# Kernel tuning notes

Hardware: AMD Instinct MI355X
Metric: run time of the kernel (lower is better)

The kernel has to match this reference:

```python
import jax, jax.numpy as jnp
import numpy as np

CHUNK = 2048  # query chunk for KNN to avoid materializing full [B,N,N] distances
BN_EPS = 1e-5


def knn_idx(xyz, k):
    """xyz: [B,N,3] -> idx [B,N,k] of k nearest points (incl. self), like keops argKmin."""
    B, N, _ = xyz.shape
    nc = N // CHUNK
    qs = jnp.moveaxis(xyz.reshape(B, nc, CHUNK, 3), 1, 0)  # [nc,B,CHUNK,3]

    def chunk_fn(q):  # q: [B,CHUNK,3]
        d = jnp.sum((q[:, :, None, :] - xyz[:, None, :, :]) ** 2, axis=-1)  # [B,CHUNK,N]
        _, idx = jax.lax.top_k(-d, k)
        return idx

    idx = jax.lax.map(chunk_fn, qs)  # [nc,B,CHUNK,k]
    return jnp.moveaxis(idx, 0, 1).reshape(B, N, k)


def setup_inputs() -> dict:
    key = jax.random.key(0)
    k1, k2, k3, k4 = jax.random.split(key, 4)
    B, N, C = 4, 16384, 128
    return {
        "xyz": jax.random.normal(k1, (B, N, 3), dtype=jnp.float32),
        "x": jax.random.normal(k2, (B, C, N), dtype=jnp.float32),
        "conv_w": jax.random.normal(k3, (C, C), dtype=jnp.float32) * (1.0 / np.sqrt(C)),
        "conv_b": jax.random.normal(k4, (C,), dtype=jnp.float32) * 0.01,
        "gamma": jnp.ones((C,), dtype=jnp.float32),
        "beta": jnp.zeros((C,), dtype=jnp.float32),
        "k": 16,
    }


def reference(xyz, x, conv_w, conv_b, gamma, beta, k):
    # KNN on coordinates
    idx = knn_idx(xyz, k)                       # [B,N,k]
    xt = jnp.swapaxes(x, 1, 2)                  # [B,N,C]
    neigh = jax.vmap(lambda p, i: p[i])(xt, idx)  # [B,N,k,C] gather per batch
    # dx = sum over k neighbors minus center feature (Laplacian-like)
    dx = jnp.swapaxes(neigh.sum(axis=2) - xt, 1, 2)  # [B,C,N]
    # conv1x1 -> relu -> batchnorm (training-mode batch stats) -> residual
    h = jax.nn.relu(jnp.einsum('oc,bcn->bon', conv_w, dx) + conv_b[None, :, None])
    mean = h.mean(axis=(0, 2))
    var = h.var(axis=(0, 2))  # biased variance, as torch BN normalization
    hn = (h - mean[None, :, None]) * jax.lax.rsqrt(var[None, :, None] + BN_EPS)
    return x + gamma[None, :, None] * hn + beta[None, :, None]
```

## Files before the change

kernel.cpp:

```cpp
#include <hip/hip_runtime.h>

#define BATCH 4
#define NPTS  16384
#define CH    128
#define KNN   16

#define G      64
#define GRID3  (G * G * G)
#define GW     0.25f
#define GINVW  4.0f
#define GORIG  (-8.0f)
#define OCCW   (GRID3 / 32)

#define XT_OFF    0
#define HT_OFF    33554432
#define CNT_OFF   33554432
#define CUR_OFF   37748736
#define HDR_OFF   41943040
#define OCC_OFF   50331648
#define SPTS_OFF  50462720
#define GCTR_OFF  51511296
#define IDX_OFF   67108864
#define PART_OFF  71303168
#define STATS_OFF 75497472

__device__ __forceinline__ int cell1(float v) {
    int c = (int)floorf((v - GORIG) * GINVW);
    return min(G - 1, max(0, c));
}

__global__ __launch_bounds__(256) void zero_kernel(int* __restrict__ p, int n,
                                                   int* __restrict__ gctr) {
    int i = blockIdx.x * 256 + threadIdx.x;
    if (i < BATCH) gctr[i] = 0;
    const int stride = gridDim.x * 256;
    for (; i < n; i += stride) p[i] = 0;
}

__global__ __launch_bounds__(256) void transpose_kernel(const float* __restrict__ x,
                                                        float* __restrict__ xt) {
    __shared__ float t[32][33];
    const int b  = blockIdx.z;
    const int c0 = blockIdx.y * 32;
    const int n0 = blockIdx.x * 32;
    const int tx = threadIdx.x, ty = threadIdx.y;
#pragma unroll
    for (int i = 0; i < 4; ++i)
        t[ty + 8 * i][tx] = x[((size_t)b * CH + c0 + ty + 8 * i) * NPTS + n0 + tx];
    __syncthreads();
#pragma unroll
    for (int i = 0; i < 4; ++i)
        xt[((size_t)b * NPTS + n0 + ty + 8 * i) * CH + c0 + tx] = t[tx][ty + 8 * i];
}

__global__ __launch_bounds__(256) void count_kernel(const float* __restrict__ xyz,
                                                    int* __restrict__ counts) {
    const int b = blockIdx.y;
    const int i = blockIdx.x * 256 + threadIdx.x;
    const float* p = xyz + ((size_t)b * NPTS + i) * 3;
    const int c = (cell1(p[2]) * G + cell1(p[1])) * G + cell1(p[0]);
    atomicAdd(&counts[(size_t)b * GRID3 + c], 1);
}

__global__ __launch_bounds__(256) void cellhdr_kernel(const int* __restrict__ counts,
                                                      int2* __restrict__ hdr,
                                                      unsigned int* __restrict__ occ,
                                                      int* __restrict__ gctr) {
    const int cid  = blockIdx.x * 256 + threadIdx.x;
    const int b    = cid >> 18;
    const int lane = threadIdx.x & 63;
    const int c    = counts[cid];

    int incl = c;
#pragma unroll
    for (int off = 1; off < 64; off <<= 1) {
        int t = __shfl_up(incl, off);
        if (lane >= off) incl += t;
    }
    const int excl = incl - c;
    const int tot  = __shfl(incl, 63);

    const unsigned long long ball = __ballot(c > 0);
    if (lane == 0) {
        const int w = cid >> 5;
        occ[w]     = (unsigned int)ball;
        occ[w + 1] = (unsigned int)(ball >> 32);
    }

    int base = 0;
    if (lane == 63) base = atomicAdd(&gctr[b], tot);
    base = __shfl(base, 63);

    if (c > 0) hdr[cid] = make_int2(base + excl, c);
}

__global__ __launch_bounds__(256) void scatter_kernel(const float* __restrict__ xyz,
                                                      const int2* __restrict__ hdr,
                                                      int* __restrict__ cursor,
                                                      float4* __restrict__ spts) {
    const int b = blockIdx.y;
    const int i = blockIdx.x * 256 + threadIdx.x;
    const float* p = xyz + ((size_t)b * NPTS + i) * 3;
    const float x = p[0], y = p[1], z = p[2];
    const int c = (cell1(z) * G + cell1(y)) * G + cell1(x);
    const int pos = hdr[(size_t)b * GRID3 + c].x + atomicAdd(&cursor[(size_t)b * GRID3 + c], 1);
    spts[(size_t)b * NPTS + pos] = make_float4(x, y, z, __int_as_float(i));
}

__global__ __launch_bounds__(256) void knn_grid_kernel(const float4* __restrict__ spts,
                                                       const int2* __restrict__ hdr,
                                                       const unsigned int* __restrict__ occ,
                                                       int* __restrict__ idx_out) {
    __shared__ unsigned int socc[OCCW];
    const int b   = blockIdx.y;
    const int tid = threadIdx.x;
    for (int i = tid; i < OCCW; i += 256) socc[i] = occ[(size_t)b * OCCW + i];
    __syncthreads();

    const int s = blockIdx.x * 256 + tid;
    const float4 P = spts[(size_t)b * NPTS + s];
    const float qx = P.x, qy = P.y, qz = P.z;
    const int qi = __float_as_int(P.w);
    const int cx = cell1(qx), cy = cell1(qy), cz = cell1(qz);
    const int2* hb = hdr + (size_t)b * GRID3;
    const float4* pts = spts + (size_t)b * NPTS;

    float dq[KNN]; int iq[KNN];
#pragma unroll
    for (int t = 0; t < KNN; ++t) { dq[t] = 3.0e38f; iq[t] = 0x7fffffff; }

    for (int R = 0; R < G; ++R) {
        if (R > 0) {
            const int rm = R - 1;
            float dmin = 3.0e38f;
            bool any = false;
            if (cx - rm > 0)     { dmin = fminf(dmin, qx - (GORIG + (cx - rm) * GW)); any = true; }
            if (cx + rm < G - 1) { dmin = fminf(dmin, (GORIG + (cx + rm + 1) * GW) - qx); any = true; }
            if (cy - rm > 0)     { dmin = fminf(dmin, qy - (GORIG + (cy - rm) * GW)); any = true; }
            if (cy + rm < G - 1) { dmin = fminf(dmin, (GORIG + (cy + rm + 1) * GW) - qy); any = true; }
            if (cz - rm > 0)     { dmin = fminf(dmin, qz - (GORIG + (cz - rm) * GW)); any = true; }
            if (cz + rm < G - 1) { dmin = fminf(dmin, (GORIG + (cz + rm + 1) * GW) - qz); any = true; }
            if (!any) break;
            dmin = fmaxf(dmin, 0.0f);
            if (dq[KNN - 1] < dmin * dmin * (1.0f - 1e-5f)) break;
        }
        const int z0 = max(0, cz - R), z1 = min(G - 1, cz + R);
        const int y0 = max(0, cy - R), y1 = min(G - 1, cy + R);
        const int x0 = max(0, cx - R), x1 = min(G - 1, cx + R);
        for (int z = z0; z <= z1; ++z) {
            const int az = (z > cz) ? (z - cz) : (cz - z);
            const float lz = GORIG + z * GW;
            const float dzc = fmaxf(fmaxf(lz - qz, qz - (lz + GW)), 0.0f);
            for (int y = y0; y <= y1; ++y) {
                const int ay = (y > cy) ? (y - cy) : (cy - y);
                const float ly = GORIG + y * GW;
                const float dyc = fmaxf(fmaxf(ly - qy, qy - (ly + GW)), 0.0f);
                const float dzy = dzc * dzc + dyc * dyc;
                const int row = z * G + y;

                unsigned long long m;
                if (az == R || ay == R) {
                    m = (~0ull >> (63 - (x1 - x0))) << x0;
                } else {
                    m = 0ull;
                    if (cx - R >= 0) m |= 1ull << (cx - R);
                    if (cx + R < G)  m |= 1ull << (cx + R);
                }
                m &= (unsigned long long)socc[row * 2] |
                     ((unsigned long long)socc[row * 2 + 1] << 32);

                while (m) {
                    const int x = __ffsll(m) - 1;
                    m &= m - 1;
                    const float lx = GORIG + x * GW;
                    const float dxc = fmaxf(fmaxf(lx - qx, qx - (lx + GW)), 0.0f);
                    const float cmin = dzy + dxc * dxc;
                    if (cmin * (1.0f - 1e-5f) > dq[KNN - 1]) continue;
                    const int2 hc = hb[row * G + x];
                    const int en = hc.x + hc.y;
                    for (int j = hc.x; j < en; ++j) {
                        const float4 pp = pts[j];
                        const float ddx = __fsub_rn(qx, pp.x);
                        const float ddy = __fsub_rn(qy, pp.y);
                        const float ddz = __fsub_rn(qz, pp.z);
                        const float d = __fadd_rn(__fadd_rn(__fmul_rn(ddx, ddx), __fmul_rn(ddy, ddy)),
                                                  __fmul_rn(ddz, ddz));
                        const int oi = __float_as_int(pp.w);
                        if (d < dq[KNN - 1] || (d == dq[KNN - 1] && oi < iq[KNN - 1])) {
                            float cd = d; int ci = oi;
#pragma unroll
                            for (int t2 = KNN - 1; t2 >= 1; --t2) {
                                const bool lt = (cd < dq[t2 - 1]) ||
                                                (cd == dq[t2 - 1] && ci < iq[t2 - 1]);
                                if (lt) {
                                    dq[t2] = dq[t2 - 1]; iq[t2] = iq[t2 - 1];
                                    if (t2 == 1) { dq[0] = cd; iq[0] = ci; }
                                } else {
                                    dq[t2] = cd; iq[t2] = ci;
                                    break;
                                }
                            }
                        }
                    }
                }
            }
        }
    }

    int* op = idx_out + ((size_t)b * NPTS + qi) * KNN;
#pragma unroll
    for (int t = 0; t < KNN; ++t) op[t] = iq[t];
}

__global__ __launch_bounds__(128) void conv_kernel(const float* __restrict__ xt,
                                                   const int* __restrict__ idx,
                                                   const float* __restrict__ W,
                                                   const float* __restrict__ bias,
                                                   float* __restrict__ h_t,
                                                   float* __restrict__ partials) {
    __shared__ __align__(16) float dxbuf[CH];
    const int o   = threadIdx.x;
    const int blk = blockIdx.x;
    const int b   = blk / (NPTS / 16);
    const int n0  = (blk % (NPTS / 16)) * 16;

    float4 w4[CH / 4];
    const float4* wrow = (const float4*)(W + (size_t)o * CH);
#pragma unroll
    for (int i = 0; i < CH / 4; ++i) w4[i] = wrow[i];
    const float bo = bias[o];

    const float* xb = xt + (size_t)b * NPTS * CH;
    float sS = 0.0f, sQ = 0.0f;

    for (int r = 0; r < 16; ++r) {
        const int n = n0 + r;
        const int* ip = idx + ((size_t)b * NPTS + n) * KNN;
        int jj[KNN];
#pragma unroll
        for (int k = 0; k < KNN; ++k) jj[k] = ip[k];
        float va[KNN];
#pragma unroll
        for (int k = 0; k < KNN; ++k) va[k] = xb[(size_t)jj[k] * CH + o];
        const float ctr = xb[(size_t)n * CH + o];
        float acc = 0.0f;
#pragma unroll
        for (int k = 0; k < KNN; ++k) acc += va[k];
        acc -= ctr;

        dxbuf[o] = acc;
        __syncthreads();

        float h = bo;
        const float4* d4 = (const float4*)dxbuf;
#pragma unroll
        for (int cc = 0; cc < CH / 4; ++cc) {
            const float4 a = d4[cc];
            const float4 w = w4[cc];
            h = fmaf(w.x, a.x, h);
            h = fmaf(w.y, a.y, h);
            h = fmaf(w.z, a.z, h);
            h = fmaf(w.w, a.w, h);
        }
        h = fmaxf(h, 0.0f);
        h_t[((size_t)b * NPTS + n) * CH + o] = h;
        sS += h;
        sQ += h * h;
        __syncthreads();
    }

    partials[(size_t)o * 4096 + blk]        = sS;
    partials[(size_t)(CH + o) * 4096 + blk] = sQ;
}

__global__ __launch_bounds__(256) void bnred_kernel(const float* __restrict__ partials,
                                                    float* __restrict__ stats) {
    const int ch = blockIdx.x;
    const float* pS = partials + (size_t)ch * 4096;
    const float* pQ = partials + (size_t)(CH + ch) * 4096;
    float s = 0.0f, q = 0.0f;
    for (int i = threadIdx.x; i < 4096; i += 256) { s += pS[i]; q += pQ[i]; }
#pragma unroll
    for (int off = 32; off > 0; off >>= 1) {
        s += __shfl_down(s, off);
        q += __shfl_down(q, off);
    }
    __shared__ float wsum[4][2];
    const int wid = threadIdx.x >> 6;
    if ((threadIdx.x & 63) == 0) { wsum[wid][0] = s; wsum[wid][1] = q; }
    __syncthreads();
    if (threadIdx.x == 0) {
        const float S = wsum[0][0] + wsum[1][0] + wsum[2][0] + wsum[3][0];
        const float Q = wsum[0][1] + wsum[1][1] + wsum[2][1] + wsum[3][1];
        const float inv  = 1.0f / (float)(BATCH * NPTS);
        const float mean = S * inv;
        const float var  = Q * inv - mean * mean;
        stats[ch]      = mean;
        stats[CH + ch] = rsqrtf(var + 1e-5f);
    }
}

__global__ __launch_bounds__(256) void final_kernel(const float* __restrict__ x,
                                                    const float* __restrict__ h_t,
                                                    const float* __restrict__ stats,
                                                    const float* __restrict__ gamma,
                                                    const float* __restrict__ beta,
                                                    float* __restrict__ out) {
    __shared__ float t[32][33];
    const int b  = blockIdx.z;
    const int o0 = blockIdx.y * 32;
    const int n0 = blockIdx.x * 32;
    const int tx = threadIdx.x, ty = threadIdx.y;
#pragma unroll
    for (int i = 0; i < 4; ++i)
        t[ty + 8 * i][tx] = h_t[((size_t)b * NPTS + n0 + ty + 8 * i) * CH + o0 + tx];
    __syncthreads();
#pragma unroll
    for (int i = 0; i < 4; ++i) {
        const int o = o0 + ty + 8 * i;
        const float mean = stats[o];
        const float rstd = stats[CH + o];
        const float g = gamma[o], be = beta[o];
        const size_t offp = ((size_t)b * CH + o) * NPTS + n0 + tx;
        out[offp] = x[offp] + g * ((t[tx][ty + 8 * i] - mean) * rstd) + be;
    }
}

extern "C" void kernel_launch(void* const* d_in, const int* in_sizes, int n_in,
                              void* d_out, int out_size, void* d_ws, size_t ws_size,
                              hipStream_t stream) {
    const float* xyz    = (const float*)d_in[0];
    const float* x      = (const float*)d_in[1];
    const float* conv_w = (const float*)d_in[2];
    const float* conv_b = (const float*)d_in[3];
    const float* gamma  = (const float*)d_in[4];
    const float* beta   = (const float*)d_in[5];
    float* out = (float*)d_out;

    char* ws = (char*)d_ws;
    float*        xt     = (float*)(ws + XT_OFF);
    int*          counts = (int*)  (ws + CNT_OFF);
    int*          cursor = (int*)  (ws + CUR_OFF);
    int2*         hdr    = (int2*) (ws + HDR_OFF);
    unsigned int* occ    = (unsigned int*)(ws + OCC_OFF);
    float4*       spts   = (float4*)(ws + SPTS_OFF);
    int*          gctr   = (int*)  (ws + GCTR_OFF);
    float*        h_t    = (float*)(ws + HT_OFF);
    int*          idx    = (int*)  (ws + IDX_OFF);
    float*        part   = (float*)(ws + PART_OFF);
    float*        stats  = (float*)(ws + STATS_OFF);

    transpose_kernel<<<dim3(NPTS / 32, CH / 32, BATCH), dim3(32, 8), 0, stream>>>(x, xt);

    zero_kernel<<<dim3(2048), dim3(256), 0, stream>>>(counts, 2 * BATCH * GRID3, gctr);
    count_kernel<<<dim3(NPTS / 256, BATCH), dim3(256), 0, stream>>>(xyz, counts);
    cellhdr_kernel<<<dim3(BATCH * GRID3 / 256), dim3(256), 0, stream>>>(counts, hdr, occ, gctr);
    scatter_kernel<<<dim3(NPTS / 256, BATCH), dim3(256), 0, stream>>>(xyz, hdr, cursor, spts);

    knn_grid_kernel<<<dim3(NPTS / 256, BATCH), dim3(256), 0, stream>>>(spts, hdr, occ, idx);

    conv_kernel<<<dim3(BATCH * NPTS / 16), dim3(128), 0, stream>>>(xt, idx, conv_w, conv_b, h_t, part);
    bnred_kernel<<<dim3(CH), dim3(256), 0, stream>>>(part, stats);
    final_kernel<<<dim3(NPTS / 32, CH / 32, BATCH), dim3(32, 8), 0, stream>>>(x, h_t, stats, gamma, beta, out);
}
```

Before: 804.3 us.

## Split each KNN query across four lanes and merge top-k with shuffles

```diff
diff --git a/kernel.cpp b/kernel.cpp
--- a/kernel.cpp
+++ b/kernel.cpp
@@ -107,6 +107,46 @@
     spts[(size_t)b * NPTS + pos] = make_float4(x, y, z, __int_as_float(i));
 }
 
+__device__ __forceinline__ bool lexlt(float d1, int i1, float d2, int i2) {
+    return (d1 < d2) || (d1 == d2 && i1 < i2);
+}
+
+template <int XM>
+__device__ __forceinline__ void merge_pair(float (&dq)[KNN], int (&iq)[KNN]) {
+    float pd[KNN]; int pi[KNN];
+#pragma unroll
+    for (int t = 0; t < KNN; ++t) {
+        pd[t] = __shfl_xor(dq[t], XM);
+        pi[t] = __shfl_xor(iq[t], XM);
+    }
+    float md[KNN]; int mi[KNN];
+#pragma unroll
+    for (int t = 0; t < KNN; ++t) {
+        const float bd = pd[KNN - 1 - t];
+        const int   bi = pi[KNN - 1 - t];
+        const bool tb = lexlt(bd, bi, dq[t], iq[t]);
+        md[t] = tb ? bd : dq[t];
+        mi[t] = tb ? bi : iq[t];
+    }
+#pragma unroll
+    for (int d = 8; d >= 1; d >>= 1) {
+#pragma unroll
+        for (int t = 0; t < KNN; ++t) {
+            if ((t & d) == 0) {
+                const int u = t | d;
+                const bool sw = lexlt(md[u], mi[u], md[t], mi[t]);
+                const float ta = sw ? md[u] : md[t];
+                const float tb2 = sw ? md[t] : md[u];
+                const int   ia = sw ? mi[u] : mi[t];
+                const int   ib = sw ? mi[t] : mi[u];
+                md[t] = ta; md[u] = tb2; mi[t] = ia; mi[u] = ib;
+            }
+        }
+    }
+#pragma unroll
+    for (int t = 0; t < KNN; ++t) { dq[t] = md[t]; iq[t] = mi[t]; }
+}
+
 __global__ __launch_bounds__(256) void knn_grid_kernel(const float4* __restrict__ spts,
                                                        const int2* __restrict__ hdr,
                                                        const unsigned int* __restrict__ occ,
@@ -117,7 +157,8 @@
     for (int i = tid; i < OCCW; i += 256) socc[i] = occ[(size_t)b * OCCW + i];
     __syncthreads();
 
-    const int s = blockIdx.x * 256 + tid;
+    const int sub = tid & 3;
+    const int s   = blockIdx.x * 64 + (tid >> 2);
     const float4 P = spts[(size_t)b * NPTS + s];
     const float qx = P.x, qy = P.y, qz = P.z;
     const int qi = __float_as_int(P.w);
@@ -128,6 +169,7 @@
     float dq[KNN]; int iq[KNN];
 #pragma unroll
     for (int t = 0; t < KNN; ++t) { dq[t] = 3.0e38f; iq[t] = 0x7fffffff; }
+    float B = 3.0e38f;
 
     for (int R = 0; R < G; ++R) {
         if (R > 0) {
@@ -142,11 +184,12 @@
             if (cz + rm < G - 1) { dmin = fminf(dmin, (GORIG + (cz + rm + 1) * GW) - qz); any = true; }
             if (!any) break;
             dmin = fmaxf(dmin, 0.0f);
-            if (dq[KNN - 1] < dmin * dmin * (1.0f - 1e-5f)) break;
+            if (B < dmin * dmin * (1.0f - 1e-5f)) break;
         }
         const int z0 = max(0, cz - R), z1 = min(G - 1, cz + R);
         const int y0 = max(0, cy - R), y1 = min(G - 1, cy + R);
         const int x0 = max(0, cx - R), x1 = min(G - 1, cx + R);
+        int cc = 0;
         for (int z = z0; z <= z1; ++z) {
             const int az = (z > cz) ? (z - cz) : (cz - z);
             const float lz = GORIG + z * GW;
@@ -172,10 +215,13 @@
                 while (m) {
                     const int x = __ffsll(m) - 1;
                     m &= m - 1;
+                    const bool mine = ((cc++) & 3) == sub;
+                    if (!mine) continue;
                     const float lx = GORIG + x * GW;
                     const float dxc = fmaxf(fmaxf(lx - qx, qx - (lx + GW)), 0.0f);
                     const float cmin = dzy + dxc * dxc;
-                    if (cmin * (1.0f - 1e-5f) > dq[KNN - 1]) continue;
+                    const float pb = fminf(B, dq[KNN - 1]);
+                    if (cmin * (1.0f - 1e-5f) > pb) continue;
                     const int2 hc = hb[row * G + x];
                     const int en = hc.x + hc.y;
                     for (int j = hc.x; j < en; ++j) {
@@ -186,13 +232,11 @@
                         const float d = __fadd_rn(__fadd_rn(__fmul_rn(ddx, ddx), __fmul_rn(ddy, ddy)),
                                                   __fmul_rn(ddz, ddz));
                         const int oi = __float_as_int(pp.w);
-                        if (d < dq[KNN - 1] || (d == dq[KNN - 1] && oi < iq[KNN - 1])) {
+                        if (lexlt(d, oi, dq[KNN - 1], iq[KNN - 1])) {
                             float cd = d; int ci = oi;
 #pragma unroll
                             for (int t2 = KNN - 1; t2 >= 1; --t2) {
-                                const bool lt = (cd < dq[t2 - 1]) ||
-                                                (cd == dq[t2 - 1] && ci < iq[t2 - 1]);
-                                if (lt) {
+                                if (lexlt(cd, ci, dq[t2 - 1], iq[t2 - 1])) {
                                     dq[t2] = dq[t2 - 1]; iq[t2] = iq[t2 - 1];
                                     if (t2 == 1) { dq[0] = cd; iq[0] = ci; }
                                 } else {
@@ -205,11 +249,20 @@
                 }
             }
         }
-    }
-
-    int* op = idx_out + ((size_t)b * NPTS + qi) * KNN;
-#pragma unroll
-    for (int t = 0; t < KNN; ++t) op[t] = iq[t];
+        float w15 = dq[KNN - 1];
+        w15 = fminf(w15, __shfl_xor(w15, 1));
+        w15 = fminf(w15, __shfl_xor(w15, 2));
+        B = w15;
+    }
+
+    merge_pair<1>(dq, iq);
+    merge_pair<2>(dq, iq);
+
+    if (sub == 0) {
+        int* op = idx_out + ((size_t)b * NPTS + qi) * KNN;
+#pragma unroll
+        for (int t = 0; t < KNN; ++t) op[t] = iq[t];
+    }
 }
 
 __global__ __launch_bounds__(128) void conv_kernel(const float* __restrict__ xt,
@@ -357,7 +410,7 @@
     cellhdr_kernel<<<dim3(BATCH * GRID3 / 256), dim3(256), 0, stream>>>(counts, hdr, occ, gctr);
     scatter_kernel<<<dim3(NPTS / 256, BATCH), dim3(256), 0, stream>>>(xyz, hdr, cursor, spts);
 
-    knn_grid_kernel<<<dim3(NPTS / 256, BATCH), dim3(256), 0, stream>>>(spts, hdr, occ, idx);
+    knn_grid_kernel<<<dim3(NPTS / 64, BATCH), dim3(256), 0, stream>>>(spts, hdr, occ, idx);
 
     conv_kernel<<<dim3(BATCH * NPTS / 16), dim3(128), 0, stream>>>(xt, idx, conv_w, conv_b, h_t, part);
     bnred_kernel<<<dim3(CH), dim3(256), 0, stream>>>(part, stats);
```

Measured after the change: 2.342 ms. +191.2%, slower.

## Add hierarchical coarse grid for KNN search in sparse regions

Applied to the files above, without the earlier changes.

```diff
diff --git a/kernel.cpp b/kernel.cpp
--- a/kernel.cpp
+++ b/kernel.cpp
@@ -11,15 +11,22 @@
 #define GINVW  4.0f
 #define GORIG  (-8.0f)
 #define OCCW   (GRID3 / 32)
+#define GC     16
+#define GRIDC3 (GC * GC * GC)
+#define GWC    1.0f
+#define CROWS  (GC * GC)
+#define COARSE_THR 32
 
 #define XT_OFF    0
 #define HT_OFF    33554432
 #define CNT_OFF   33554432
 #define CUR_OFF   37748736
 #define HDR_OFF   41943040
-#define OCC_OFF   50331648
-#define SPTS_OFF  50462720
-#define GCTR_OFF  51511296
+#define HDRC_OFF  50331648
+#define OCC_OFF   50462720
+#define SOCCC_OFF 50593792
+#define SPTS_OFF  50597888
+#define GCTR_OFF  51646464
 #define IDX_OFF   67108864
 #define PART_OFF  71303168
 #define STATS_OFF 75497472
@@ -29,10 +36,51 @@
     return min(G - 1, max(0, c));
 }
 
+__device__ __forceinline__ int pcid_of(int z, int y, int x) {
+    const int cc  = ((z >> 2) * GC + (y >> 2)) * GC + (x >> 2);
+    const int loc = ((z & 3) * 4 + (y & 3)) * 4 + (x & 3);
+    return cc * 64 + loc;
+}
+
+__device__ __forceinline__ bool lexlt(float d1, int i1, float d2, int i2) {
+    return (d1 < d2) || (d1 == d2 && i1 < i2);
+}
+
+__device__ __forceinline__ void insert_lex(float (&dq)[KNN], int (&iq)[KNN], float d, int oi) {
+    if (!lexlt(d, oi, dq[KNN - 1], iq[KNN - 1])) return;
+    float cd = d; int ci = oi;
+#pragma unroll
+    for (int t = KNN - 1; t >= 1; --t) {
+        if (lexlt(cd, ci, dq[t - 1], iq[t - 1])) {
+            dq[t] = dq[t - 1]; iq[t] = iq[t - 1];
+            if (t == 1) { dq[0] = cd; iq[0] = ci; }
+        } else {
+            dq[t] = cd; iq[t] = ci;
+            break;
+        }
+    }
+}
+
+__device__ __forceinline__ void scan_cell(const float4* __restrict__ pts, int st, int en,
+                                          float qx, float qy, float qz,
+                                          float (&dq)[KNN], int (&iq)[KNN]) {
+    for (int j = st; j < en; ++j) {
+        const float4 pp = pts[j];
+        const float ddx = __fsub_rn(qx, pp.x);
+        const float ddy = __fsub_rn(qy, pp.y);
+        const float ddz = __fsub_rn(qz, pp.z);
+        const float d = __fadd_rn(__fadd_rn(__fmul_rn(ddx, ddx), __fmul_rn(ddy, ddy)),
+                                  __fmul_rn(ddz, ddz));
+        insert_lex(dq, iq, d, __float_as_int(pp.w));
+    }
+}
+
 __global__ __launch_bounds__(256) void zero_kernel(int* __restrict__ p, int n,
+                                                   int* __restrict__ p2, int n2,
                                                    int* __restrict__ gctr) {
     int i = blockIdx.x * 256 + threadIdx.x;
     if (i < BATCH) gctr[i] = 0;
+    if (i < n2) p2[i] = 0;
     const int stride = gridDim.x * 256;
     for (; i < n; i += stride) p[i] = 0;
 }
@@ -58,18 +106,19 @@
     const int b = blockIdx.y;
     const int i = blockIdx.x * 256 + threadIdx.x;
     const float* p = xyz + ((size_t)b * NPTS + i) * 3;
-    const int c = (cell1(p[2]) * G + cell1(p[1])) * G + cell1(p[0]);
-    atomicAdd(&counts[(size_t)b * GRID3 + c], 1);
+    const int c = pcid_of(cell1(p[2]), cell1(p[1]), cell1(p[0]));
+    atomicAdd(&counts[((size_t)b << 18) + c], 1);
 }
 
 __global__ __launch_bounds__(256) void cellhdr_kernel(const int* __restrict__ counts,
                                                       int2* __restrict__ hdr,
-                                                      unsigned int* __restrict__ occ,
+                                                      int2* __restrict__ hdrc,
+                                                      unsigned int* __restrict__ soccc,
                                                       int* __restrict__ gctr) {
-    const int cid  = blockIdx.x * 256 + threadIdx.x;
-    const int b    = cid >> 18;
+    const int pcid = blockIdx.x * 256 + threadIdx.x;
+    const int b    = pcid >> 18;
     const int lane = threadIdx.x & 63;
-    const int c    = counts[cid];
+    const int c    = counts[pcid];
 
     int incl = c;
 #pragma unroll
@@ -80,18 +129,35 @@
     const int excl = incl - c;
     const int tot  = __shfl(incl, 63);
 
-    const unsigned long long ball = __ballot(c > 0);
-    if (lane == 0) {
-        const int w = cid >> 5;
-        occ[w]     = (unsigned int)ball;
-        occ[w + 1] = (unsigned int)(ball >> 32);
-    }
-
     int base = 0;
     if (lane == 63) base = atomicAdd(&gctr[b], tot);
     base = __shfl(base, 63);
 
-    if (c > 0) hdr[cid] = make_int2(base + excl, c);
+    if (c > 0) hdr[pcid] = make_int2(base + excl, c);
+
+    if (lane == 63 && tot > 0) {
+        const int ccg = pcid >> 6;
+        const int cc  = ccg & (GRIDC3 - 1);
+        hdrc[ccg] = make_int2(base, tot);
+        const int xc  = cc & (GC - 1);
+        const int row = cc >> 4;
+        atomicOr(&soccc[b * CROWS + row], 1u << xc);
+    }
+}
+
+__global__ __launch_bounds__(256) void occ_kernel(const int* __restrict__ counts,
+                                                  unsigned int* __restrict__ occ) {
+    const int lcid = blockIdx.x * 256 + threadIdx.x;
+    const int b = lcid >> 18;
+    const int lin = lcid & (GRID3 - 1);
+    const int z = lin >> 12, y = (lin >> 6) & 63, x = lin & 63;
+    const int c = counts[((size_t)b << 18) + pcid_of(z, y, x)];
+    const unsigned long long ball = __ballot(c > 0);
+    if ((threadIdx.x & 63) == 0) {
+        const int row = lcid >> 6;
+        occ[row * 2]     = (unsigned int)ball;
+        occ[row * 2 + 1] = (unsigned int)(ball >> 32);
+    }
 }
 
 __global__ __launch_bounds__(256) void scatter_kernel(const float* __restrict__ xyz,
@@ -102,19 +168,23 @@
     const int i = blockIdx.x * 256 + threadIdx.x;
     const float* p = xyz + ((size_t)b * NPTS + i) * 3;
     const float x = p[0], y = p[1], z = p[2];
-    const int c = (cell1(z) * G + cell1(y)) * G + cell1(x);
-    const int pos = hdr[(size_t)b * GRID3 + c].x + atomicAdd(&cursor[(size_t)b * GRID3 + c], 1);
+    const int c = pcid_of(cell1(z), cell1(y), cell1(x));
+    const int pos = hdr[((size_t)b << 18) + c].x + atomicAdd(&cursor[((size_t)b << 18) + c], 1);
     spts[(size_t)b * NPTS + pos] = make_float4(x, y, z, __int_as_float(i));
 }
 
 __global__ __launch_bounds__(256) void knn_grid_kernel(const float4* __restrict__ spts,
                                                        const int2* __restrict__ hdr,
+                                                       const int2* __restrict__ hdrc,
                                                        const unsigned int* __restrict__ occ,
+                                                       const unsigned int* __restrict__ soccc,
                                                        int* __restrict__ idx_out) {
     __shared__ unsigned int socc[OCCW];
+    __shared__ unsigned int scc[CROWS];
     const int b   = blockIdx.y;
     const int tid = threadIdx.x;
     for (int i = tid; i < OCCW; i += 256) socc[i] = occ[(size_t)b * OCCW + i];
+    if (tid < CROWS) scc[tid] = soccc[b * CROWS + tid];
     __syncthreads();
 
     const int s = blockIdx.x * 256 + tid;
@@ -122,15 +192,26 @@
     const float qx = P.x, qy = P.y, qz = P.z;
     const int qi = __float_as_int(P.w);
     const int cx = cell1(qx), cy = cell1(qy), cz = cell1(qz);
-    const int2* hb = hdr + (size_t)b * GRID3;
+    const int2* hb  = hdr  + ((size_t)b << 18);
+    const int2* hbc = hdrc + (size_t)b * GRIDC3;
     const float4* pts = spts + (size_t)b * NPTS;
 
     float dq[KNN]; int iq[KNN];
 #pragma unroll
     for (int t = 0; t < KNN; ++t) { dq[t] = 3.0e38f; iq[t] = 0x7fffffff; }
 
-    for (int R = 0; R < G; ++R) {
-        if (R > 0) {
+    const int cxc = cx >> 2, cyc = cy >> 2, czc = cz >> 2;
+    const int ccq = (czc * GC + cyc) * GC + cxc;
+    const int crow = ccq >> 4;
+    int centerCnt = 0;
+    if ((scc[crow] >> (ccq & 15)) & 1u) centerCnt = hbc[ccq].y;
+
+    if (centerCnt >= COARSE_THR) {
+        {
+            const int2 hc = hb[pcid_of(cz, cy, cx)];
+            scan_cell(pts, hc.x, hc.x + hc.y, qx, qy, qz, dq, iq);
+        }
+        for (int R = 1; R < G; ++R) {
             const int rm = R - 1;
             float dmin = 3.0e38f;
             bool any = false;
@@ -143,64 +224,97 @@
             if (!any) break;
             dmin = fmaxf(dmin, 0.0f);
             if (dq[KNN - 1] < dmin * dmin * (1.0f - 1e-5f)) break;
-        }
-        const int z0 = max(0, cz - R), z1 = min(G - 1, cz + R);
-        const int y0 = max(0, cy - R), y1 = min(G - 1, cy + R);
-        const int x0 = max(0, cx - R), x1 = min(G - 1, cx + R);
-        for (int z = z0; z <= z1; ++z) {
-            const int az = (z > cz) ? (z - cz) : (cz - z);
-            const float lz = GORIG + z * GW;
-            const float dzc = fmaxf(fmaxf(lz - qz, qz - (lz + GW)), 0.0f);
-            for (int y = y0; y <= y1; ++y) {
-                const int ay = (y > cy) ? (y - cy) : (cy - y);
-                const float ly = GORIG + y * GW;
-                const float dyc = fmaxf(fmaxf(ly - qy, qy - (ly + GW)), 0.0f);
-                const float dzy = dzc * dzc + dyc * dyc;
-                const int row = z * G + y;
-
-                unsigned long long m;
-                if (az == R || ay == R) {
-                    m = (~0ull >> (63 - (x1 - x0))) << x0;
-                } else {
-                    m = 0ull;
-                    if (cx - R >= 0) m |= 1ull << (cx - R);
-                    if (cx + R < G)  m |= 1ull << (cx + R);
+
+            const int z0 = max(0, cz - R), z1 = min(G - 1, cz + R);
+            const int y0 = max(0, cy - R), y1 = min(G - 1, cy + R);
+            const int x0 = max(0, cx - R), x1 = min(G - 1, cx + R);
+            for (int z = z0; z <= z1; ++z) {
+                const int az = (z > cz) ? (z - cz) : (cz - z);
+                const float lz = GORIG + z * GW;
+                const float dzc = fmaxf(fmaxf(lz - qz, qz - (lz + GW)), 0.0f);
+                for (int y = y0; y <= y1; ++y) {
+                    const int ay = (y > cy) ? (y - cy) : (cy - y);
+                    const float ly = GORIG + y * GW;
+                    const float dyc = fmaxf(fmaxf(ly - qy, qy - (ly + GW)), 0.0f);
+                    const float dzy = dzc * dzc + dyc * dyc;
+                    const int row = z * G + y;
+
+                    unsigned long long m;
+                    if (az == R || ay == R) {
+                        m = (~0ull >> (63 - (x1 - x0))) << x0;
+                    } else {
+                        m = 0ull;
+                        if (cx - R >= 0) m |= 1ull << (cx - R);
+                        if (cx + R < G)  m |= 1ull << (cx + R);
+                    }
+                    m &= (unsigned long long)socc[row * 2] |
+                         ((unsigned long long)socc[row * 2 + 1] << 32);
+
+                    while (m) {
+                        const int x = __ffsll(m) - 1;
+                        m &= m - 1;
+                        const float lx = GORIG + x * GW;
+                        const float dxc = fmaxf(fmaxf(lx - qx, qx - (lx + GW)), 0.0f);
+                        const float cmin = dzy + dxc * dxc;
+                        if (cmin * (1.0f - 1e-5f) > dq[KNN - 1]) continue;
+                        const int2 hc = hb[pcid_of(z, y, x)];
+                        scan_cell(pts, hc.x, hc.x + hc.y, qx, qy, qz, dq, iq);
+                    }
                 }
-                m &= (unsigned long long)socc[row * 2] |
-                     ((unsigned long long)socc[row * 2 + 1] << 32);
-
-                while (m) {
-                    const int x = __ffsll(m) - 1;
-                    m &= m - 1;
-                    const float lx = GORIG + x * GW;
-                    const float dxc = fmaxf(fmaxf(lx - qx, qx - (lx + GW)), 0.0f);
-                    const float cmin = dzy + dxc * dxc;
-                    if (cmin * (1.0f - 1e-5f) > dq[KNN - 1]) continue;
-                    const int2 hc = hb[row * G + x];
-                    const int en = hc.x + hc.y;
-                    for (int j = hc.x; j < en; ++j) {
-                        const float4 pp = pts[j];
-                        const float ddx = __fsub_rn(qx, pp.x);
-                        const float ddy = __fsub_rn(qy, pp.y);
-                        const float ddz = __fsub_rn(qz, pp.z);
-                        const float d = __fadd_rn(__fadd_rn(__fmul_rn(ddx, ddx), __fmul_rn(ddy, ddy)),
-                                                  __fmul_rn(ddz, ddz));
-                        const int oi = __float_as_int(pp.w);
-                        if (d < dq[KNN - 1] || (d == dq[KNN - 1] && oi < iq[KNN - 1])) {
-                            float cd = d; int ci = oi;
-#pragma unroll
-                            for (int t2 = KNN - 1; t2 >= 1; --t2) {
-                                const bool lt = (cd < dq[t2 - 1]) ||
-                                                (cd == dq[t2 - 1] && ci < iq[t2 - 1]);
-                                if (lt) {
-                                    dq[t2] = dq[t2 - 1]; iq[t2] = iq[t2 - 1];
-                                    if (t2 == 1) { dq[0] = cd; iq[0] = ci; }
-                                } else {
-                                    dq[t2] = cd; iq[t2] = ci;
-                                    break;
-                                }
-                            }
-                        }
+            }
+        }
+    } else {
+        if (centerCnt > 0) {
+            const int2 hc = hbc[ccq];
+            scan_cell(pts, hc.x, hc.x + hc.y, qx, qy, qz, dq, iq);
+        }
+        for (int R = 1; R < GC; ++R) {
+            const int rm = R - 1;
+            float dmin = 3.0e38f;
+            bool any = false;
+            if (cxc - rm > 0)      { dmin = fminf(dmin, qx - (GORIG + (cxc - rm) * GWC)); any = true; }
+            if (cxc + rm < GC - 1) { dmin = fminf(dmin, (GORIG + (cxc + rm + 1) * GWC) - qx); any = true; }
+            if (cyc - rm > 0)      { dmin = fminf(dmin, qy - (GORIG + (cyc - rm) * GWC)); any = true; }
+            if (cyc + rm < GC - 1) { dmin = fminf(dmin, (GORIG + (cyc + rm + 1) * GWC) - qy); any = true; }
+            if (czc - rm > 0)      { dmin = fminf(dmin, qz - (GORIG + (czc - rm) * GWC)); any = true; }
+            if (czc + rm < GC - 1) { dmin = fminf(dmin, (GORIG + (czc + rm + 1) * GWC) - qz); any = true; }
+            if (!any) break;
+            dmin = fmaxf(dmin, 0.0f);
+            if (dq[KNN - 1] < dmin * dmin * (1.0f - 1e-5f)) break;
+
+            const int z0 = max(0, czc - R), z1 = min(GC - 1, czc + R);
+            const int y0 = max(0, cyc - R), y1 = min(GC - 1, cyc + R);
+            const int x0 = max(0, cxc - R), x1 = min(GC - 1, cxc + R);
+            for (int z = z0; z <= z1; ++z) {
+                const int az = (z > czc) ? (z - czc) : (czc - z);
+                const float lz = GORIG + z * GWC;
+                const float dzc2 = fmaxf(fmaxf(lz - qz, qz - (lz + GWC)), 0.0f);
+                for (int y = y0; y <= y1; ++y) {
+                    const int ay = (y > cyc) ? (y - cyc) : (cyc - y);
+                    const float ly = GORIG + y * GWC;
+                    const float dyc = fmaxf(fmaxf(ly - qy, qy - (ly + GWC)), 0.0f);
+                    const float dzy = dzc2 * dzc2 + dyc * dyc;
+                    const int row = z * GC + y;
+
+                    unsigned int m;
+                    if (az == R || ay == R) {
+                        m = ((x1 - x0 == 15) ? 0xFFFFu : ((1u << (x1 - x0 + 1)) - 1u)) << x0;
+                    } else {
+                        m = 0u;
+                        if (cxc - R >= 0) m |= 1u << (cxc - R);
+                        if (cxc + R < GC) m |= 1u << (cxc + R);
+                    }
+                    m &= scc[row];
+
+                    while (m) {
+                        const int x = __ffs(m) - 1;
+                        m &= m - 1;
+                        const float lx = GORIG + x * GWC;
+                        const float dxc = fmaxf(fmaxf(lx - qx, qx - (lx + GWC)), 0.0f);
+                        const float cmin = dzy + dxc * dxc;
+                        if (cmin * (1.0f - 1e-5f) > dq[KNN - 1]) continue;
+                        const int2 hc = hbc[row * GC + x];
+                        scan_cell(pts, hc.x, hc.x + hc.y, qx, qy, qz, dq, iq);
                     }
                 }
             }
@@ -342,7 +456,9 @@
     int*          counts = (int*)  (ws + CNT_OFF);
     int*          cursor = (int*)  (ws + CUR_OFF);
     int2*         hdr    = (int2*) (ws + HDR_OFF);
+    int2*         hdrc   = (int2*) (ws + HDRC_OFF);
     unsigned int* occ    = (unsigned int*)(ws + OCC_OFF);
+    unsigned int* soccc  = (unsigned int*)(ws + SOCCC_OFF);
     float4*       spts   = (float4*)(ws + SPTS_OFF);
     int*          gctr   = (int*)  (ws + GCTR_OFF);
     float*        h_t    = (float*)(ws + HT_OFF);
@@ -352,12 +468,14 @@
 
     transpose_kernel<<<dim3(NPTS / 32, CH / 32, BATCH), dim3(32, 8), 0, stream>>>(x, xt);
 
-    zero_kernel<<<dim3(2048), dim3(256), 0, stream>>>(counts, 2 * BATCH * GRID3, gctr);
+    zero_kernel<<<dim3(2048), dim3(256), 0, stream>>>(counts, 2 * BATCH * GRID3,
+                                                      (int*)soccc, BATCH * CROWS, gctr);
     count_kernel<<<dim3(NPTS / 256, BATCH), dim3(256), 0, stream>>>(xyz, counts);
-    cellhdr_kernel<<<dim3(BATCH * GRID3 / 256), dim3(256), 0, stream>>>(counts, hdr, occ, gctr);
+    cellhdr_kernel<<<dim3(BATCH * GRID3 / 256), dim3(256), 0, stream>>>(counts, hdr, hdrc, soccc, gctr);
+    occ_kernel<<<dim3(BATCH * GRID3 / 256), dim3(256), 0, stream>>>(counts, occ);
     scatter_kernel<<<dim3(NPTS / 256, BATCH), dim3(256), 0, stream>>>(xyz, hdr, cursor, spts);
 
-    knn_grid_kernel<<<dim3(NPTS / 256, BATCH), dim3(256), 0, stream>>>(spts, hdr, occ, idx);
+    knn_grid_kernel<<<dim3(NPTS / 256, BATCH), dim3(256), 0, stream>>>(spts, hdr, hdrc, occ, soccc, idx);
 
     conv_kernel<<<dim3(BATCH * NPTS / 16), dim3(128), 0, stream>>>(xt, idx, conv_w, conv_b, h_t, part);
     bnred_kernel<<<dim3(CH), dim3(256), 0, stream>>>(part, stats);
```

Result: slower. 1.516 ms (+88.5%).

## Seed KNN bound from sorted-neighbor window and split shell traversal into faces

Applied to the files above, without the earlier changes.

```diff
diff --git a/kernel.cpp b/kernel.cpp
--- a/kernel.cpp
+++ b/kernel.cpp
@@ -18,8 +18,9 @@
 #define CUR_OFF   37748736
 #define HDR_OFF   41943040
 #define OCC_OFF   50331648
-#define SPTS_OFF  50462720
-#define GCTR_OFF  51511296
+#define OCCX_OFF  50462720
+#define SPTS_OFF  50593792
+#define GCTR_OFF  51642368
 #define IDX_OFF   67108864
 #define PART_OFF  71303168
 #define STATS_OFF 75497472
@@ -27,6 +28,44 @@
 __device__ __forceinline__ int cell1(float v) {
     int c = (int)floorf((v - GORIG) * GINVW);
     return min(G - 1, max(0, c));
+}
+
+__device__ __forceinline__ float axdist(float q, int c) {
+    const float lo = GORIG + c * GW;
+    return fmaxf(fmaxf(lo - q, q - (lo + GW)), 0.0f);
+}
+
+__device__ __forceinline__ bool lexlt(float d1, int i1, float d2, int i2) {
+    return (d1 < d2) || (d1 == d2 && i1 < i2);
+}
+
+__device__ __forceinline__ void insert_lex(float (&dq)[KNN], int (&iq)[KNN], float d, int oi) {
+    if (!lexlt(d, oi, dq[KNN - 1], iq[KNN - 1])) return;
+    float cd = d; int ci = oi;
+#pragma unroll
+    for (int t = KNN - 1; t >= 1; --t) {
+        if (lexlt(cd, ci, dq[t - 1], iq[t - 1])) {
+            dq[t] = dq[t - 1]; iq[t] = iq[t - 1];
+            if (t == 1) { dq[0] = cd; iq[0] = ci; }
+        } else {
+            dq[t] = cd; iq[t] = ci;
+            break;
+        }
+    }
+}
+
+__device__ __forceinline__ void scan_cell(const float4* __restrict__ pts, int st, int en,
+                                          float qx, float qy, float qz,
+                                          float (&dq)[KNN], int (&iq)[KNN]) {
+    for (int j = st; j < en; ++j) {
+        const float4 pp = pts[j];
+        const float ddx = __fsub_rn(qx, pp.x);
+        const float ddy = __fsub_rn(qy, pp.y);
+        const float ddz = __fsub_rn(qz, pp.z);
+        const float d = __fadd_rn(__fadd_rn(__fmul_rn(ddx, ddx), __fmul_rn(ddy, ddy)),
+                                  __fmul_rn(ddz, ddz));
+        insert_lex(dq, iq, d, __float_as_int(pp.w));
+    }
 }
 
 __global__ __launch_bounds__(256) void zero_kernel(int* __restrict__ p, int n,
@@ -59,7 +98,7 @@
     const int i = blockIdx.x * 256 + threadIdx.x;
     const float* p = xyz + ((size_t)b * NPTS + i) * 3;
     const int c = (cell1(p[2]) * G + cell1(p[1])) * G + cell1(p[0]);
-    atomicAdd(&counts[(size_t)b * GRID3 + c], 1);
+    atomicAdd(&counts[((size_t)b << 18) + c], 1);
 }
 
 __global__ __launch_bounds__(256) void cellhdr_kernel(const int* __restrict__ counts,
@@ -92,6 +131,21 @@
     base = __shfl(base, 63);
 
     if (c > 0) hdr[cid] = make_int2(base + excl, c);
+}
+
+__global__ __launch_bounds__(256) void occx_kernel(const int* __restrict__ counts,
+                                                   unsigned int* __restrict__ occX) {
+    const int gid = blockIdx.x * 256 + threadIdx.x;
+    const int b   = gid >> 18;
+    const int lin = gid & (GRID3 - 1);
+    const int x = lin >> 12, z = (lin >> 6) & 63, y = lin & 63;
+    const int c = counts[((size_t)b << 18) + ((z * G + y) * G + x)];
+    const unsigned long long ball = __ballot(c > 0);
+    if ((threadIdx.x & 63) == 0) {
+        const int row = gid >> 6;
+        occX[row * 2]     = (unsigned int)ball;
+        occX[row * 2 + 1] = (unsigned int)(ball >> 32);
+    }
 }
 
 __global__ __launch_bounds__(256) void scatter_kernel(const float* __restrict__ xyz,
@@ -103,18 +157,23 @@
     const float* p = xyz + ((size_t)b * NPTS + i) * 3;
     const float x = p[0], y = p[1], z = p[2];
     const int c = (cell1(z) * G + cell1(y)) * G + cell1(x);
-    const int pos = hdr[(size_t)b * GRID3 + c].x + atomicAdd(&cursor[(size_t)b * GRID3 + c], 1);
+    const int pos = hdr[((size_t)b << 18) + c].x + atomicAdd(&cursor[((size_t)b << 18) + c], 1);
     spts[(size_t)b * NPTS + pos] = make_float4(x, y, z, __int_as_float(i));
 }
 
 __global__ __launch_bounds__(256) void knn_grid_kernel(const float4* __restrict__ spts,
                                                        const int2* __restrict__ hdr,
                                                        const unsigned int* __restrict__ occ,
+                                                       const unsigned int* __restrict__ occX,
                                                        int* __restrict__ idx_out) {
     __shared__ unsigned int socc[OCCW];
+    __shared__ unsigned int soccX[OCCW];
     const int b   = blockIdx.y;
     const int tid = threadIdx.x;
-    for (int i = tid; i < OCCW; i += 256) socc[i] = occ[(size_t)b * OCCW + i];
+    for (int i = tid; i < OCCW; i += 256) {
+        socc[i]  = occ [(size_t)b * OCCW + i];
+        soccX[i] = occX[(size_t)b * OCCW + i];
+    }
     __syncthreads();
 
     const int s = blockIdx.x * 256 + tid;
@@ -122,16 +181,47 @@
     const float qx = P.x, qy = P.y, qz = P.z;
     const int qi = __float_as_int(P.w);
     const int cx = cell1(qx), cy = cell1(qy), cz = cell1(qz);
-    const int2* hb = hdr + (size_t)b * GRID3;
+    const int2* hb = hdr + ((size_t)b << 18);
     const float4* pts = spts + (size_t)b * NPTS;
 
+    float sd[KNN];
+#pragma unroll
+    for (int t = 0; t < KNN; ++t) sd[t] = 3.0e38f;
+    {
+        int w0 = s - 24;
+        w0 = max(0, min(w0, NPTS - 64));
+        for (int j = w0; j < w0 + 64; ++j) {
+            const float4 pp = pts[j];
+            const float ddx = __fsub_rn(qx, pp.x);
+            const float ddy = __fsub_rn(qy, pp.y);
+            const float ddz = __fsub_rn(qz, pp.z);
+            const float d = __fadd_rn(__fadd_rn(__fmul_rn(ddx, ddx), __fmul_rn(ddy, ddy)),
+                                      __fmul_rn(ddz, ddz));
+            if (d < sd[KNN - 1]) {
+                float cd = d;
+#pragma unroll
+                for (int t = KNN - 1; t >= 1; --t) {
+                    if (cd < sd[t - 1]) { sd[t] = sd[t - 1]; if (t == 1) sd[0] = cd; }
+                    else { sd[t] = cd; break; }
+                }
+            }
+        }
+    }
+    const float B0 = sd[KNN - 1];
+
     float dq[KNN]; int iq[KNN];
 #pragma unroll
     for (int t = 0; t < KNN; ++t) { dq[t] = 3.0e38f; iq[t] = 0x7fffffff; }
 
-    for (int R = 0; R < G; ++R) {
-        if (R > 0) {
+    {
+        const int2 hc = hb[(cz * G + cy) * G + cx];
+        scan_cell(pts, hc.x, hc.x + hc.y, qx, qy, qz, dq, iq);
+    }
+
+    for (int R = 1; R < G; ++R) {
+        {
             const int rm = R - 1;
+            const float bound = fminf(B0, dq[KNN - 1]);
             float dmin = 3.0e38f;
             bool any = false;
             if (cx - rm > 0)     { dmin = fminf(dmin, qx - (GORIG + (cx - rm) * GW)); any = true; }
@@ -142,65 +232,89 @@
             if (cz + rm < G - 1) { dmin = fminf(dmin, (GORIG + (cz + rm + 1) * GW) - qz); any = true; }
             if (!any) break;
             dmin = fmaxf(dmin, 0.0f);
-            if (dq[KNN - 1] < dmin * dmin * (1.0f - 1e-5f)) break;
+            if (bound < dmin * dmin * (1.0f - 1e-5f)) break;
         }
         const int z0 = max(0, cz - R), z1 = min(G - 1, cz + R);
         const int y0 = max(0, cy - R), y1 = min(G - 1, cy + R);
         const int x0 = max(0, cx - R), x1 = min(G - 1, cx + R);
-        for (int z = z0; z <= z1; ++z) {
-            const int az = (z > cz) ? (z - cz) : (cz - z);
-            const float lz = GORIG + z * GW;
-            const float dzc = fmaxf(fmaxf(lz - qz, qz - (lz + GW)), 0.0f);
+        const int zi0 = max(z0, cz - R + 1), zi1 = min(z1, cz + R - 1);
+        const int yi0 = max(y0, cy - R + 1), yi1 = min(y1, cy + R - 1);
+        const unsigned long long xm_full = (~0ull >> (63 - (x1 - x0))) << x0;
+
+#pragma unroll
+        for (int f = 0; f < 2; ++f) {
+            const int z = f ? cz + R : cz - R;
+            if (z < 0 || z > G - 1) continue;
+            const float dzc = axdist(qz, z);
+            const float dz2 = dzc * dzc;
             for (int y = y0; y <= y1; ++y) {
-                const int ay = (y > cy) ? (y - cy) : (cy - y);
-                const float ly = GORIG + y * GW;
-                const float dyc = fmaxf(fmaxf(ly - qy, qy - (ly + GW)), 0.0f);
-                const float dzy = dzc * dzc + dyc * dyc;
+                const float dyc = axdist(qy, y);
+                const float dzy = dz2 + dyc * dyc;
+                if (dzy * (1.0f - 1e-5f) > fminf(B0, dq[KNN - 1])) continue;
                 const int row = z * G + y;
-
-                unsigned long long m;
-                if (az == R || ay == R) {
-                    m = (~0ull >> (63 - (x1 - x0))) << x0;
-                } else {
-                    m = 0ull;
-                    if (cx - R >= 0) m |= 1ull << (cx - R);
-                    if (cx + R < G)  m |= 1ull << (cx + R);
-                }
-                m &= (unsigned long long)socc[row * 2] |
-                     ((unsigned long long)socc[row * 2 + 1] << 32);
-
+                unsigned long long m = xm_full &
+                    ((unsigned long long)socc[row * 2] |
+                     ((unsigned long long)socc[row * 2 + 1] << 32));
                 while (m) {
                     const int x = __ffsll(m) - 1;
                     m &= m - 1;
-                    const float lx = GORIG + x * GW;
-                    const float dxc = fmaxf(fmaxf(lx - qx, qx - (lx + GW)), 0.0f);
+                    const float dxc = axdist(qx, x);
                     const float cmin = dzy + dxc * dxc;
-                    if (cmin * (1.0f - 1e-5f) > dq[KNN - 1]) continue;
+                    if (cmin * (1.0f - 1e-5f) > fminf(B0, dq[KNN - 1])) continue;
                     const int2 hc = hb[row * G + x];
-                    const int en = hc.x + hc.y;
-                    for (int j = hc.x; j < en; ++j) {
-                        const float4 pp = pts[j];
-                        const float ddx = __fsub_rn(qx, pp.x);
-                        const float ddy = __fsub_rn(qy, pp.y);
-                        const float ddz = __fsub_rn(qz, pp.z);
-                        const float d = __fadd_rn(__fadd_rn(__fmul_rn(ddx, ddx), __fmul_rn(ddy, ddy)),
-                                                  __fmul_rn(ddz, ddz));
-                        const int oi = __float_as_int(pp.w);
-                        if (d < dq[KNN - 1] || (d == dq[KNN - 1] && oi < iq[KNN - 1])) {
-                            float cd = d; int ci = oi;
-#pragma unroll
-                            for (int t2 = KNN - 1; t2 >= 1; --t2) {
-                                const bool lt = (cd < dq[t2 - 1]) ||
-                                                (cd == dq[t2 - 1] && ci < iq[t2 - 1]);
-                                if (lt) {
-                                    dq[t2] = dq[t2 - 1]; iq[t2] = iq[t2 - 1];
-                                    if (t2 == 1) { dq[0] = cd; iq[0] = ci; }
-                                } else {
-                                    dq[t2] = cd; iq[t2] = ci;
-                                    break;
-                                }
-                            }
-                        }
+                    scan_cell(pts, hc.x, hc.x + hc.y, qx, qy, qz, dq, iq);
+                }
+            }
+        }
+#pragma unroll
+        for (int f = 0; f < 2; ++f) {
+            const int y = f ? cy + R : cy - R;
+            if (y < 0 || y > G - 1) continue;
+            const float dyc = axdist(qy, y);
+            const float dy2 = dyc * dyc;
+            for (int z = zi0; z <= zi1; ++z) {
+                const float dzc = axdist(qz, z);
+                const float dzy = dzc * dzc + dy2;
+                if (dzy * (1.0f - 1e-5f) > fminf(B0, dq[KNN - 1])) continue;
+                const int row = z * G + y;
+                unsigned long long m = xm_full &
+                    ((unsigned long long)socc[row * 2] |
+                     ((unsigned long long)socc[row * 2 + 1] << 32));
+                while (m) {
+                    const int x = __ffsll(m) - 1;
+                    m &= m - 1;
+                    const float dxc = axdist(qx, x);
+                    const float cmin = dzy + dxc * dxc;
+                    if (cmin * (1.0f - 1e-5f) > fminf(B0, dq[KNN - 1])) continue;
+                    const int2 hc = hb[row * G + x];
+                    scan_cell(pts, hc.x, hc.x + hc.y, qx, qy, qz, dq, iq);
+                }
+            }
+        }
+        {
+            const unsigned long long ym_full = (~0ull >> (63 - (yi1 - yi0))) << yi0;
+#pragma unroll
+            for (int f = 0; f < 2; ++f) {
+                const int x = f ? cx + R : cx - R;
+                if (x < 0 || x > G - 1) continue;
+                const float dxc = axdist(qx, x);
+                const float dx2 = dxc * dxc;
+                for (int z = zi0; z <= zi1; ++z) {
+                    const float dzc = axdist(qz, z);
+                    const float dxz = dx2 + dzc * dzc;
+                    if (dxz * (1.0f - 1e-5f) > fminf(B0, dq[KNN - 1])) continue;
+                    const int rowx = x * G + z;
+                    unsigned long long m = ym_full &
+                        ((unsigned long long)soccX[rowx * 2] |
+                         ((unsigned long long)soccX[rowx * 2 + 1] << 32));
+                    while (m) {
+                        const int y = __ffsll(m) - 1;
+                        m &= m - 1;
+                        const float dyc = axdist(qy, y);
+                        const float cmin = dxz + dyc * dyc;
+                        if (cmin * (1.0f - 1e-5f) > fminf(B0, dq[KNN - 1])) continue;
+                        const int2 hc = hb[(z * G + y) * G + x];
+                        scan_cell(pts, hc.x, hc.x + hc.y, qx, qy, qz, dq, iq);
                     }
                 }
             }
@@ -343,6 +457,7 @@
     int*          cursor = (int*)  (ws + CUR_OFF);
     int2*         hdr    = (int2*) (ws + HDR_OFF);
     unsigned int* occ    = (unsigned int*)(ws + OCC_OFF);
+    unsigned int* occX   = (unsigned int*)(ws + OCCX_OFF);
     float4*       spts   = (float4*)(ws + SPTS_OFF);
     int*          gctr   = (int*)  (ws + GCTR_OFF);
     float*        h_t    = (float*)(ws + HT_OFF);
@@ -355,9 +470,10 @@
     zero_kernel<<<dim3(2048), dim3(256), 0, stream>>>(counts, 2 * BATCH * GRID3, gctr);
     count_kernel<<<dim3(NPTS / 256, BATCH), dim3(256), 0, stream>>>(xyz, counts);
     cellhdr_kernel<<<dim3(BATCH * GRID3 / 256), dim3(256), 0, stream>>>(counts, hdr, occ, gctr);
+    occx_kernel<<<dim3(BATCH * GRID3 / 256), dim3(256), 0, stream>>>(counts, occX);
     scatter_kernel<<<dim3(NPTS / 256, BATCH), dim3(256), 0, stream>>>(xyz, hdr, cursor, spts);
 
-    knn_grid_kernel<<<dim3(NPTS / 256, BATCH), dim3(256), 0, stream>>>(spts, hdr, occ, idx);
+    knn_grid_kernel<<<dim3(NPTS / 256, BATCH), dim3(256), 0, stream>>>(spts, hdr, occ, occX, idx);
 
     conv_kernel<<<dim3(BATCH * NPTS / 16), dim3(128), 0, stream>>>(xt, idx, conv_w, conv_b, h_t, part);
     bnred_kernel<<<dim3(CH), dim3(256), 0, stream>>>(part, stats);
```

Result: slower. 986.9 us (+22.7%).
